# Optimization experiments

Measured on AMD Instinct MI355X. Metric: run time of the kernel, lower is better.

## Reference

```python
import jax, jax.numpy as jnp
import numpy as np
import math

DN = ('NCHW', 'OIHW', 'NCHW')

def conv3x3(x, w, b):
    # 3x3, stride 1, SAME padding conv with bias, NCHW layout
    y = jax.lax.conv_general_dilated(x, w, window_strides=(1, 1), padding='SAME', dimension_numbers=DN)
    return y + b[None, :, None, None]

def setup_inputs() -> dict:
    key = jax.random.key(0)
    ks = jax.random.split(key, 12)
    B, C, NC, S = 16, 256, 80, 4  # batch, fpn channels, num_classes, stem depth
    std = 0.01
    inp = {}
    inp['feat_p3'] = jax.random.normal(ks[0], (B, C, 64, 64), jnp.float32)
    inp['feat_p4'] = jax.random.normal(ks[1], (B, C, 32, 32), jnp.float32)
    inp['feat_p5'] = jax.random.normal(ks[2], (B, C, 16, 16), jnp.float32)
    # stem conv stacks: (S, out_c, in_c, 3, 3); all channels equal so stacking is valid
    inp['stem_cls_w'] = std * jax.random.normal(ks[3], (S, C, C, 3, 3), jnp.float32)
    inp['stem_cls_b'] = jnp.zeros((S, C), jnp.float32)
    inp['stem_box_w'] = std * jax.random.normal(ks[4], (S, C, C, 3, 3), jnp.float32)
    inp['stem_box_b'] = jnp.zeros((S, C), jnp.float32)
    inp['pred_cls_w'] = std * jax.random.normal(ks[5], (NC, C, 3, 3), jnp.float32)
    inp['pred_cls_b'] = jnp.full((NC,), -math.log(99.0), jnp.float32)  # prior-prob bias init
    inp['pred_box_w'] = std * jax.random.normal(ks[6], (4, C, 3, 3), jnp.float32)
    inp['pred_box_b'] = jnp.zeros((4,), jnp.float32)
    inp['pred_ctr_w'] = std * jax.random.normal(ks[7], (1, C, 3, 3), jnp.float32)
    inp['pred_ctr_b'] = jnp.zeros((1,), jnp.float32)
    return inp

def _flatten_hw(t):
    # (B, Ch, H, W) -> (B, H*W, Ch), channels-last as in the torch module
    B, Ch, H, W = t.shape
    return t.transpose(0, 2, 3, 1).reshape(B, H * W, Ch)

def reference(feat_p3, feat_p4, feat_p5, stem_cls_w, stem_cls_b, stem_box_w, stem_box_b,
              pred_cls_w, pred_cls_b, pred_box_w, pred_box_b, pred_ctr_w, pred_ctr_b):
    per_level = []
    for feat in (feat_p3, feat_p4, feat_p5):
        cls_feat = feat
        box_feat = feat
        for i in range(stem_cls_w.shape[0]):  # fixed small stem depth (4)
            cls_feat = jax.nn.relu(conv3x3(cls_feat, stem_cls_w[i], stem_cls_b[i]))
            box_feat = jax.nn.relu(conv3x3(box_feat, stem_box_w[i], stem_box_b[i]))
        cls_logits = conv3x3(cls_feat, pred_cls_w, pred_cls_b)   # (B, 80, H, W)
        box_deltas = conv3x3(box_feat, pred_box_w, pred_box_b)   # (B, 4, H, W)
        ctr_logits = conv3x3(box_feat, pred_ctr_w, pred_ctr_b)   # (B, 1, H, W)
        per_level.append(jnp.concatenate(
            [_flatten_hw(cls_logits), _flatten_hw(box_deltas), _flatten_hw(ctr_logits)], axis=-1))
    # concat p3/p4/p5 along location axis -> (B, 4096+1024+256, 85)
    return jnp.concatenate(per_level, axis=1)
```

## Files before the change

### kernel.cpp

```cpp
#include <hip/hip_runtime.h>


typedef __bf16 bf16;
typedef __attribute__((ext_vector_type(8))) __bf16 bf16x8;
typedef __attribute__((ext_vector_type(4))) float f32x4;

typedef unsigned int uint32_as1 __attribute__((address_space(1)));
typedef unsigned int uint32_as3 __attribute__((address_space(3)));

__device__ __forceinline__ void gl_lds16(const bf16* g, bf16* l) {
    __builtin_amdgcn_global_load_lds(
        (const uint32_as1*)(unsigned long long)g,
        (uint32_as3*)(unsigned int)(unsigned long long)l,
        16, 0, 0);
}

struct StemTab {
    const bf16* inC[3]; const bf16* inB[3];
    bf16* outC[3]; bf16* outB[3];
    int H[3]; int lw[3]; int lhw[3];
    int xend0, xend1;
};
struct PredTab {
    const bf16* inC[3]; const bf16* inB[3];
    int H[3]; int lw[3]; int lhw[3]; int offl[3];
    int xend0, xend1;
};
struct CastTab {
    const float* in[3]; bf16* out[3];
    int H[3]; int lw[3];
    int xend0, xend1;
};
struct BZTab {
    bf16* base[3]; int H[3]; size_t bufE[3]; int ppi[3];
    int xend0, xend1;
};

__global__ __launch_bounds__(256) void stem_conv_kernel(
    StemTab tab, const bf16* __restrict__ Wc, const bf16* __restrict__ Wb,
    const float* __restrict__ bc, const float* __restrict__ bb)
{
    const int bx = blockIdx.x;
    const int l  = (bx >= tab.xend0) + (bx >= tab.xend1);
    const int start = (l == 0) ? 0 : (l == 1 ? tab.xend0 : tab.xend1);
    const int local = bx - start;
    const int H = tab.H[l], lw = tab.lw[l], lhw = tab.lhw[l];

    const bf16* A; bf16* O; const bf16* BT; const float* bias;
    if (blockIdx.z == 0) { A = tab.inC[l]; O = tab.outC[l]; BT = Wc; bias = bc; }
    else                 { A = tab.inB[l]; O = tab.outB[l]; BT = Wb; bias = bb; }

    const int W   = 1 << lw;
    const int Wp  = W + 2;
    const int HW  = 1 << lhw;
    const int tid = threadIdx.x;
    const int m_base = (local >> 1) * 128;
    const int n0     = (local & 1) * 128;
    const int b   = m_base >> lhw;
    const int y0  = (m_base & (HW - 1)) >> lw;
    const int ibase = b * (H + 2) * Wp * 256;

    __shared__ __align__(16) bf16 Sh[26624];
    bf16* Als = Sh;
    bf16* Bls = Sh + 10240;

    const int ch8   = (((tid & 7) ^ ((tid >> 3) & 7)) << 3);
    const int rbase = tid >> 3;
    const int Wp256 = Wp * 256;
    const int npx   = (128 >> lw) * Wp;
    const int toff  = (128 + rbase < npx) ? 4 * 8192 : 0;
    const int ag0   = ibase + rbase * 256 + ch8;
    int bg[4];
#pragma unroll
    for (int i = 0; i < 4; ++i)
        bg[i] = (n0 + i * 32 + rbase) * 256 + ch8;

    f32x4 acc[4][4];
#pragma unroll
    for (int i = 0; i < 4; ++i)
#pragma unroll
        for (int j = 0; j < 4; ++j)
            acc[i][j] = (f32x4)(0.0f);

    const int lane = tid & 63;
    const int wv   = tid >> 6;
    const int wm   = (wv & 1) * 64;
    const int wn   = (wv >> 1) * 64;
    const int l16  = lane & 15;
    const int quad = lane >> 4;
    int pb[4];
#pragma unroll
    for (int i = 0; i < 4; ++i) {
        const int mm = wm + i * 16;
        pb[i] = mm + ((mm >> lw) << 1) + l16;
    }
    const int bRow = (wn + l16) * 64;
    const int bsw  = l16 & 7;
    bf16* const lA = Als + tid * 8;
    bf16* const lB = Bls + tid * 8;

    auto stageA = [&](int dy, int cq) {
        const int abase = ag0 + (y0 + dy) * Wp256 + (cq << 6);
#pragma unroll
        for (int i = 0; i < 4; ++i)
            gl_lds16(A + abase + i * 8192, lA + i * 2048);
        gl_lds16(A + abase + toff, lA + 4 * 2048);
    };
    auto stageB = [&](int half, int tap, int cq) {
        const int boff = tap * 65536 + (cq << 6);
        bf16* dst = lB + half * 8192;
#pragma unroll
        for (int i = 0; i < 4; ++i)
            gl_lds16(BT + bg[i] + boff, dst + i * 2048);
    };

    stageB(0, 0, 0);
    int curb = 0;

    for (int dy = 0; dy < 3; ++dy)
        for (int cq = 0; cq < 4; ++cq) {
            stageA(dy, cq);
#pragma unroll
            for (int dx = 0; dx < 3; ++dx) {
                int ndy = dy, ncq = cq, ndx = dx + 1;
                if (ndx == 3) { ndx = 0; if (++ncq == 4) { ncq = 0; ++ndy; } }
                const bool more = (ndy < 3);
                if (more) {
                    stageB(curb ^ 1, ndy * 3 + ndx, ncq);
                    asm volatile("s_waitcnt vmcnt(4)" ::: "memory");
                } else {
                    asm volatile("s_waitcnt vmcnt(0)" ::: "memory");
                }
                __builtin_amdgcn_s_barrier();
                __builtin_amdgcn_sched_barrier(0);
                const bf16* Bc = Bls + curb * 8192;
                int rowi[4];
#pragma unroll
                for (int i = 0; i < 4; ++i) rowi[i] = pb[i] + dx;
#pragma unroll
                for (int ks = 0; ks < 2; ++ks) {
                    const int qk = quad + ks * 4;
                    bf16x8 af[4], bfv[4];
#pragma unroll
                    for (int i = 0; i < 4; ++i)
                        af[i] = *(const bf16x8*)(Als + (rowi[i] << 6) +
                                                 ((qk ^ (rowi[i] & 7)) << 3));
#pragma unroll
                    for (int j = 0; j < 4; ++j)
                        bfv[j] = *(const bf16x8*)(Bc + bRow + j * 1024 +
                                                  ((qk ^ bsw) << 3));
#pragma unroll
                    for (int i = 0; i < 4; ++i)
#pragma unroll
                        for (int j = 0; j < 4; ++j)
                            acc[i][j] = __builtin_amdgcn_mfma_f32_16x16x32_bf16(
                                af[i], bfv[j], acc[i][j], 0, 0, 0);
                }
                __builtin_amdgcn_sched_barrier(0);
                __builtin_amdgcn_s_barrier();
                curb ^= 1;
            }
        }

    float bv[4];
#pragma unroll
    for (int j = 0; j < 4; ++j) bv[j] = bias[n0 + wn + j * 16 + l16];
    bf16* Tw = Sh + wv * 4096;
#pragma unroll
    for (int i = 0; i < 4; ++i)
#pragma unroll
        for (int r = 0; r < 4; ++r) {
            const int row = i * 16 + quad * 4 + r;
#pragma unroll
            for (int j = 0; j < 4; ++j) {
                float v = acc[i][j][r] + bv[j];
                v = v > 0.0f ? v : 0.0f;
                const int sc = (((j * 2 + (l16 >> 3)) ^ (row & 7)) << 3) + (l16 & 7);
                Tw[row * 64 + sc] = (bf16)v;
            }
        }
    __syncthreads();
    const int rgrp = lane >> 3, cc = lane & 7;
#pragma unroll
    for (int p = 0; p < 8; ++p) {
        const int row = p * 8 + rgrp;
        bf16x8 vv = *(const bf16x8*)(Tw + row * 64 + ((cc ^ (row & 7)) << 3));
        const int ml = wm + row;
        const int y  = y0 + (ml >> lw);
        const int x  = ml & (W - 1);
        *(bf16x8*)(O + ibase + ((y + 1) * Wp + (x + 1)) * 256 + n0 + wn + cc * 8) = vv;
    }
}

__global__ __launch_bounds__(256) void pred_conv_kernel(
    PredTab tab, const bf16* __restrict__ BT, const float* __restrict__ bias,
    float* __restrict__ out)
{
    const int bx = blockIdx.x;
    const int l  = (bx >= tab.xend0) + (bx >= tab.xend1);
    const int start = (l == 0) ? 0 : (l == 1 ? tab.xend0 : tab.xend1);
    const int mt = bx - start;
    const int H = tab.H[l], lw = tab.lw[l], lhw = tab.lhw[l], off_l = tab.offl[l];
    const bf16* Ac = tab.inC[l];
    const bf16* Ab = tab.inB[l];

    const int W   = 1 << lw;
    const int Wp  = W + 2;
    const int HW  = 1 << lhw;
    const int tid = threadIdx.x;
    const int m_base = mt * 128;
    const int b   = m_base >> lhw;
    const int mi  = m_base & (HW - 1);
    const int y0  = mi >> lw;
    const int ibase = b * (H + 2) * Wp * 256;

    __shared__ __align__(16) bf16 Sh[(128 + 128 + 96) * 64];

    const int ch8   = (((tid & 7) ^ ((tid >> 3) & 7)) << 3);
    const int rbase = tid >> 3;
    int ag[4], bg[3];
#pragma unroll
    for (int i = 0; i < 4; ++i) {
        int row = i * 32 + rbase;
        int y = y0 + (row >> lw);
        int x = row & (W - 1);
        ag[i] = ibase + (y * Wp + x) * 256 + ch8;
    }
#pragma unroll
    for (int i = 0; i < 3; ++i)
        bg[i] = (i * 32 + rbase) * 256 + ch8;

    f32x4 accC[2][5], accB[2];
#pragma unroll
    for (int i = 0; i < 2; ++i) {
#pragma unroll
        for (int j = 0; j < 5; ++j) accC[i][j] = (f32x4)(0.0f);
        accB[i] = (f32x4)(0.0f);
    }

    const int lane = tid & 63;
    const int wv   = tid >> 6;
    const int l16  = lane & 15;
    const int quad = lane >> 4;
    const int xsw  = l16 & 7;
    const int aRow = (wv * 32 + l16) * 64;
    bf16* lS = Sh + tid * 8;

    for (int kc = 0; kc < 36; ++kc) {
        const int t  = kc >> 2;
        const int dy = t / 3;
        const int dx = t - dy * 3;
        const int c0 = (kc & 3) << 6;
        const int aoff = (dy * Wp + dx) * 256 + c0;
        const int boff = t * 24576 + c0;
#pragma unroll
        for (int i = 0; i < 4; ++i)
            gl_lds16(Ac + ag[i] + aoff, lS + i * 2048);
#pragma unroll
        for (int i = 0; i < 4; ++i)
            gl_lds16(Ab + ag[i] + aoff, lS + (4 + i) * 2048);
#pragma unroll
        for (int i = 0; i < 3; ++i)
            gl_lds16(BT + bg[i] + boff, lS + (8 + i) * 2048);
        __syncthreads();
#pragma unroll
        for (int ks = 0; ks < 2; ++ks) {
            const int cO = (((quad + ks * 4) ^ xsw) << 3);
            bf16x8 afc[2], afb[2], bfv[5], bfb;
#pragma unroll
            for (int i = 0; i < 2; ++i) {
                afc[i] = *(const bf16x8*)(Sh + aRow + i * 1024 + cO);
                afb[i] = *(const bf16x8*)(Sh + 8192 + aRow + i * 1024 + cO);
            }
#pragma unroll
            for (int j = 0; j < 5; ++j)
                bfv[j] = *(const bf16x8*)(Sh + 16384 + (j * 16 + l16) * 64 + cO);
            bfb = *(const bf16x8*)(Sh + 16384 + (80 + l16) * 64 + cO);
#pragma unroll
            for (int i = 0; i < 2; ++i) {
#pragma unroll
                for (int j = 0; j < 5; ++j)
                    accC[i][j] = __builtin_amdgcn_mfma_f32_16x16x32_bf16(
                        afc[i], bfv[j], accC[i][j], 0, 0, 0);
                accB[i] = __builtin_amdgcn_mfma_f32_16x16x32_bf16(
                    afb[i], bfb, accB[i], 0, 0, 0);
            }
        }
        __syncthreads();
    }

#pragma unroll
    for (int i = 0; i < 2; ++i) {
#pragma unroll
        for (int r = 0; r < 4; ++r) {
            const int ml  = wv * 32 + i * 16 + quad * 4 + r;
            const int pos = mi + ml;
            const int ob  = (b * 5376 + off_l + pos) * 85;
#pragma unroll
            for (int j = 0; j < 5; ++j)
                out[ob + j * 16 + l16] = accC[i][j][r] + bias[j * 16 + l16];
            if (l16 < 5)
                out[ob + 80 + l16] = accB[i][r] + bias[80 + l16];
        }
    }
}

__global__ __launch_bounds__(256) void cast_pad_kernel(CastTab tb)
{
    const int bx = blockIdx.x;
    const int l  = (bx >= tb.xend0) + (bx >= tb.xend1);
    const int start = (l == 0) ? 0 : (l == 1 ? tb.xend0 : tb.xend1);
    const int job = bx - start;
    const int H = tb.H[l], lw = tb.lw[l];
    const int W = 1 << lw, Wp = W + 2;
    const int b = job >> lw;
    const int y = job & (W - 1);
    const float* in = tb.in[l] + ((size_t)(b * 256) * H + y) * W;
    bf16* out = tb.out[l] + ((size_t)(b * (H + 2) + y + 1) * Wp + 1) * 256;
    const int tid = threadIdx.x;
    __shared__ bf16 L[16384];
    const int cpp = 256 >> lw;
    const int x = tid & (W - 1);
    const int cb0 = tid >> lw;
    for (int p = 0; p < W; ++p) {
        const int c = p * cpp + cb0;
        float v = in[(size_t)c * H * W + x];
        L[x * 256 + ((((c >> 3) ^ (x & 31))) << 3) + (c & 7)] = (bf16)v;
    }
    __syncthreads();
    const int wpass = W >> 3;
    for (int q = 0; q < wpass; ++q) {
        const int id = q * 256 + tid;
        const int xo = id >> 5;
        const int k  = id & 31;
        bf16x8 vv = *(const bf16x8*)(L + xo * 256 + ((k ^ (xo & 31)) << 3));
        *(bf16x8*)(out + xo * 256 + k * 8) = vv;
    }
}

__global__ void border_zero_kernel(BZTab tb)
{
    const int bx = blockIdx.x;
    const int l  = (bx >= tb.xend0) + (bx >= tb.xend1);
    const int start = (l == 0) ? 0 : (l == 1 ? tb.xend0 : tb.xend1);
    const int i   = bx - start;
    const int buf = blockIdx.y;
    const int c   = threadIdx.x;
    const int H = tb.H[l];
    const int ppi = tb.ppi[l];
    const int img = i / ppi;
    const int p   = i - img * ppi;
    const int Wp  = H + 2, Hp = H + 2;
    int y, xp;
    if (p < Wp)            { y = 0;      xp = p; }
    else if (p < 2 * Wp)   { y = Hp - 1; xp = p - Wp; }
    else { int q = p - 2 * Wp; y = 1 + (q >> 1); xp = (q & 1) ? (Wp - 1) : 0; }
    tb.base[l][buf * tb.bufE[l] + ((size_t)(img * Hp + y) * Wp + xp) * 256 + c]
        = (bf16)0.0f;
}

__global__ void prepack_kernel(const float* __restrict__ scw,
                               const float* __restrict__ sbw,
                               const float* __restrict__ pcw,
                               const float* __restrict__ pbw,
                               const float* __restrict__ prw,
                               const float* __restrict__ pcb,
                               const float* __restrict__ pbb,
                               const float* __restrict__ prb,
                               bf16* __restrict__ wc, bf16* __restrict__ wb,
                               bf16* __restrict__ pT, float* __restrict__ pB)
{
    const int ci = threadIdx.x;
    int g = blockIdx.x;
    if (g < 18432) {
        const float* w = (g < 9216) ? scw : sbw;
        bf16* o        = (g < 9216) ? wc  : wb;
        if (g >= 9216) g -= 9216;
        const int co = g & 255;
        const int st = g >> 8;
        const int s  = st / 9;
        const int t  = st - s * 9;
        o[(size_t)g * 256 + ci] = (bf16)w[(((s * 256 + co) * 256 + ci) * 9) + t];
    } else {
        g -= 18432;
        const int t  = g / 96;
        const int co = g - t * 96;
        float v = 0.0f;
        if (co < 80)       v = pcw[((co * 256 + ci) * 9) + t];
        else if (co < 84)  v = pbw[(((co - 80) * 256 + ci) * 9) + t];
        else if (co == 84) v = prw[(ci * 9) + t];
        pT[(size_t)g * 256 + ci] = (bf16)v;
        if (g == 0 && ci < 96) {
            float bvv = 0.0f;
            if (ci < 80)       bvv = pcb[ci];
            else if (ci < 84)  bvv = pbb[ci - 80];
            else if (ci == 84) bvv = prb[0];
            pB[ci] = bvv;
        }
    }
}

extern "C" void kernel_launch(void* const* d_in, const int* in_sizes, int n_in,
                              void* d_out, int out_size, void* d_ws, size_t ws_size,
                              hipStream_t stream)
{
    (void)in_sizes; (void)n_in; (void)out_size;
    const float* feat[3] = {(const float*)d_in[0], (const float*)d_in[1],
                            (const float*)d_in[2]};
    const float* scw = (const float*)d_in[3];
    const float* scb = (const float*)d_in[4];
    const float* sbw = (const float*)d_in[5];
    const float* sbb = (const float*)d_in[6];
    const float* pcw = (const float*)d_in[7];
    const float* pcb = (const float*)d_in[8];
    const float* pbw = (const float*)d_in[9];
    const float* pbb = (const float*)d_in[10];
    const float* prw = (const float*)d_in[11];
    const float* prb = (const float*)d_in[12];
    float* out = (float*)d_out;

    const int Hs[3]   = {64, 32, 16};
    const int lws[3]  = {6, 5, 4};
    const int lhws[3] = {12, 10, 8};
    const int offl[3] = {0, 4096, 5120};
    const int mtiles[3] = {512, 128, 32};
    size_t bufB[3];
    for (int l = 0; l < 3; ++l)
        bufB[l] = (size_t)16 * (Hs[l] + 2) * (Hs[l] + 2) * 256 * 2;

    const size_t WSTEM = (size_t)4 * 9 * 256 * 256 * 2;
    const size_t WPRED = (size_t)9 * 96 * 256 * 2;
    const size_t FULL   = 5 * (bufB[0] + bufB[1] + bufB[2]) + 2 * WSTEM + WPRED + 384;
    const size_t SHARED = 5 * bufB[0] + 2 * WSTEM + WPRED + 384;
    if (ws_size < SHARED) return;
    const bool fused = ws_size >= FULL;

    char* ws = (char*)d_ws;
    bf16* act[3][5];
    size_t off = 0;
    if (fused) {
        for (int l = 0; l < 3; ++l)
            for (int k = 0; k < 5; ++k) { act[l][k] = (bf16*)(ws + off); off += bufB[l]; }
    } else {
        for (int k = 0; k < 5; ++k)
            for (int l = 0; l < 3; ++l) act[l][k] = (bf16*)(ws + (size_t)k * bufB[0]);
        off = 5 * bufB[0];
    }
    bf16*  wbTc = (bf16*)(ws + off); off += WSTEM;
    bf16*  wbTb = (bf16*)(ws + off); off += WSTEM;
    bf16*  pT   = (bf16*)(ws + off); off += WPRED;
    float* pB   = (float*)(ws + off);

    prepack_kernel<<<dim3(19296), 256, 0, stream>>>(scw, sbw, pcw, pbw, prw,
                                                    pcb, pbb, prb,
                                                    wbTc, wbTb, pT, pB);

    auto make_stem_tab = [&](int s, int nlev, const int* levs) {
        StemTab tb{};
        for (int i = 0; i < nlev; ++i) {
            int l = levs[i];
            tb.inC[i]  = (s == 0) ? act[l][0] : ((s & 1) ? act[l][1] : act[l][2]);
            tb.inB[i]  = (s == 0) ? act[l][0] : ((s & 1) ? act[l][3] : act[l][4]);
            tb.outC[i] = (s & 1) ? act[l][2] : act[l][1];
            tb.outB[i] = (s & 1) ? act[l][4] : act[l][3];
            tb.H[i] = Hs[l]; tb.lw[i] = lws[l]; tb.lhw[i] = lhws[l];
        }
        return tb;
    };

    if (fused) {
        BZTab bz{};
        int bpx[3];
        for (int l = 0; l < 3; ++l) {
            bz.base[l] = act[l][0]; bz.H[l] = Hs[l]; bz.bufE[l] = bufB[l] / 2;
            bpx[l] = 2 * (Hs[l] + 2) + 2 * Hs[l];
            bz.ppi[l] = bpx[l];
        }
        bz.xend0 = 16 * bpx[0]; bz.xend1 = bz.xend0 + 16 * bpx[1];
        const int bztot = bz.xend1 + 16 * bpx[2];
        border_zero_kernel<<<dim3(bztot, 5), 256, 0, stream>>>(bz);

        CastTab ct{};
        for (int l = 0; l < 3; ++l) {
            ct.in[l] = feat[l]; ct.out[l] = act[l][0];
            ct.H[l] = Hs[l]; ct.lw[l] = lws[l];
        }
        ct.xend0 = 16 * Hs[0]; ct.xend1 = ct.xend0 + 16 * Hs[1];
        cast_pad_kernel<<<dim3(ct.xend1 + 16 * Hs[2]), 256, 0, stream>>>(ct);

        const int levs[3] = {0, 1, 2};
        const int tx0 = mtiles[0] * 2, tx1 = mtiles[1] * 2, tx2 = mtiles[2] * 2;
        for (int s = 0; s < 4; ++s) {
            StemTab tb = make_stem_tab(s, 3, levs);
            tb.xend0 = tx0; tb.xend1 = tx0 + tx1;
            stem_conv_kernel<<<dim3(tx0 + tx1 + tx2, 1, 2), 256, 0, stream>>>(
                tb, wbTc + (size_t)s * 589824, wbTb + (size_t)s * 589824,
                scb + s * 256, sbb + s * 256);
        }
        PredTab pt{};
        for (int l = 0; l < 3; ++l) {
            pt.inC[l] = act[l][2]; pt.inB[l] = act[l][4];
            pt.H[l] = Hs[l]; pt.lw[l] = lws[l]; pt.lhw[l] = lhws[l]; pt.offl[l] = offl[l];
        }
        pt.xend0 = mtiles[0]; pt.xend1 = mtiles[0] + mtiles[1];
        pred_conv_kernel<<<dim3(mtiles[0] + mtiles[1] + mtiles[2]), 256, 0, stream>>>(
            pt, pT, pB, out);
    } else {
        for (int l = 0; l < 3; ++l) {
            const int bpx = 2 * (Hs[l] + 2) + 2 * Hs[l];
            BZTab bz{};
            bz.base[0] = act[l][0]; bz.H[0] = Hs[l]; bz.bufE[0] = bufB[0] / 2;
            bz.ppi[0] = bpx; bz.xend0 = 16 * bpx; bz.xend1 = 16 * bpx;
            border_zero_kernel<<<dim3(16 * bpx, 5), 256, 0, stream>>>(bz);
            CastTab ct{};
            ct.in[0] = feat[l]; ct.out[0] = act[l][0];
            ct.H[0] = Hs[l]; ct.lw[0] = lws[l];
            ct.xend0 = 16 * Hs[l]; ct.xend1 = 16 * Hs[l];
            cast_pad_kernel<<<dim3(16 * Hs[l]), 256, 0, stream>>>(ct);

            const int levs[1] = {l};
            const int tiles = mtiles[l] * 2;
            for (int s = 0; s < 4; ++s) {
                StemTab tb = make_stem_tab(s, 1, levs);
                tb.xend0 = tiles; tb.xend1 = tiles;
                stem_conv_kernel<<<dim3(tiles, 1, 2), 256, 0, stream>>>(
                    tb, wbTc + (size_t)s * 589824, wbTb + (size_t)s * 589824,
                    scb + s * 256, sbb + s * 256);
            }
            PredTab pt{};
            pt.inC[0] = act[l][2]; pt.inB[0] = act[l][4];
            pt.H[0] = Hs[l]; pt.lw[0] = lws[l]; pt.lhw[0] = lhws[l]; pt.offl[0] = offl[l];
            pt.xend0 = mtiles[l]; pt.xend1 = mtiles[l];
            pred_conv_kernel<<<dim3(mtiles[l]), 256, 0, stream>>>(pt, pT, pB, out);
        }
    }
}
```

Measured before the change: 1.032 ms.

## Prefetch weight tiles through registers with a single LDS buffer instead of double-buffered LDS

The weight (B) tile for the next tap is now loaded from global memory into registers before the MFMA loop and written to one LDS buffer after a barrier, replacing the double-buffered direct global-to-LDS loads. The A tile is also staged after the compute step instead of before it. LDS use drops from 26624 to 18432 bf16 elements, which may allow more resident blocks per CU. The cost is extra VGPRs for the prefetch registers and an extra barrier per step, while the A staging now has no overlap with compute.

```diff
diff --git a/kernel.cpp b/kernel.cpp
--- a/kernel.cpp
+++ b/kernel.cpp
@@ -60,7 +60,7 @@
     const int y0  = (m_base & (HW - 1)) >> lw;
     const int ibase = b * (H + 2) * Wp * 256;
 
-    __shared__ __align__(16) bf16 Sh[26624];
+    __shared__ __align__(16) bf16 Sh[18432];
     bf16* Als = Sh;
     bf16* Bls = Sh + 10240;
 
@@ -106,34 +106,34 @@
             gl_lds16(A + abase + i * 8192, lA + i * 2048);
         gl_lds16(A + abase + toff, lA + 4 * 2048);
     };
-    auto stageB = [&](int half, int tap, int cq) {
+
+    bf16x8 breg[4];
+    auto loadB = [&](int tap, int cq) {
         const int boff = tap * 65536 + (cq << 6);
-        bf16* dst = lB + half * 8192;
 #pragma unroll
         for (int i = 0; i < 4; ++i)
-            gl_lds16(BT + bg[i] + boff, dst + i * 2048);
+            breg[i] = *(const bf16x8*)(BT + bg[i] + boff);
     };
-
-    stageB(0, 0, 0);
-    int curb = 0;
+    auto writeB = [&]() {
+#pragma unroll
+        for (int i = 0; i < 4; ++i)
+            *(bf16x8*)(lB + i * 2048) = breg[i];
+    };
+
+    stageA(0, 0);
+    loadB(0, 0);
+    writeB();
+    __syncthreads();
 
     for (int dy = 0; dy < 3; ++dy)
         for (int cq = 0; cq < 4; ++cq) {
-            stageA(dy, cq);
 #pragma unroll
             for (int dx = 0; dx < 3; ++dx) {
                 int ndy = dy, ncq = cq, ndx = dx + 1;
                 if (ndx == 3) { ndx = 0; if (++ncq == 4) { ncq = 0; ++ndy; } }
                 const bool more = (ndy < 3);
-                if (more) {
-                    stageB(curb ^ 1, ndy * 3 + ndx, ncq);
-                    asm volatile("s_waitcnt vmcnt(4)" ::: "memory");
-                } else {
-                    asm volatile("s_waitcnt vmcnt(0)" ::: "memory");
-                }
-                __builtin_amdgcn_s_barrier();
+                if (more) loadB(ndy * 3 + ndx, ncq);
                 __builtin_amdgcn_sched_barrier(0);
-                const bf16* Bc = Bls + curb * 8192;
                 int rowi[4];
 #pragma unroll
                 for (int i = 0; i < 4; ++i) rowi[i] = pb[i] + dx;
@@ -147,7 +147,7 @@
                                                  ((qk ^ (rowi[i] & 7)) << 3));
 #pragma unroll
                     for (int j = 0; j < 4; ++j)
-                        bfv[j] = *(const bf16x8*)(Bc + bRow + j * 1024 +
+                        bfv[j] = *(const bf16x8*)(Bls + bRow + j * 1024 +
                                                   ((qk ^ bsw) << 3));
 #pragma unroll
                     for (int i = 0; i < 4; ++i)
@@ -158,7 +158,12 @@
                 }
                 __builtin_amdgcn_sched_barrier(0);
                 __builtin_amdgcn_s_barrier();
-                curb ^= 1;
+                __builtin_amdgcn_sched_barrier(0);
+                if (more) {
+                    if (ndx == 0) stageA(ndy, ncq);
+                    writeB();
+                    __syncthreads();
+                }
             }
         }
 
```

New measurement: 1.100 ms. 1.07x slower.
